# Kernel tuning notes

Measured on AMD Instinct MI355X. Metric: run time of the kernel, lower is better.

Reference implementation:

```python
import jax, jax.numpy as jnp
import numpy as np

K_HOPS = 2


def setup_inputs() -> dict:
    key = jax.random.key(0)
    k1, k2, k3 = jax.random.split(key, 3)
    N, E, D, C = 100000, 3200000, 512, 40
    x = jax.random.normal(k1, (N, D), dtype=jnp.float32)
    edge_index = jax.random.randint(k2, (2, E), 0, N, dtype=jnp.int64)
    W = jax.random.normal(k3, (C, D), dtype=jnp.float32) * 0.05
    b = jnp.zeros((C,), dtype=jnp.float32)
    return {"x": x, "edge_index": edge_index, "W": W, "b": b}


def reference(x, edge_index, W, b):
    # SGConv: K-hop symmetric-normalized propagation, then Linear, then log_softmax.
    # Dropout is identity at inference (training=False).
    N = x.shape[0]
    loop = jnp.arange(N, dtype=edge_index.dtype)
    src = jnp.concatenate([edge_index[0], loop])  # source nodes (+ self-loops)
    dst = jnp.concatenate([edge_index[1], loop])  # target nodes (+ self-loops)
    ew = jnp.ones(src.shape[0], dtype=x.dtype)
    # deg^{-1/2} A_hat deg^{-1/2}: degree computed at the target (col) index, as in PyG gcn_norm
    deg = jax.ops.segment_sum(ew, dst, num_segments=N)
    dinv = jnp.where(deg > 0, jax.lax.rsqrt(deg), 0.0)
    norm = dinv[src] * dinv[dst]  # [E+N]
    h = x
    for _ in range(K_HOPS):
        # gather source features, weight, scatter-add to targets
        h = jax.ops.segment_sum(norm[:, None] * h[src], dst, num_segments=N)
    logits = h @ W.T + b  # [N, C]
    return jax.nn.log_softmax(logits, axis=1)
```

## Files before the change

### kernel.cpp

```cpp
#include <hip/hip_runtime.h>
#include <hip/hip_bf16.h>


#define TPB 256
#define ETILE 16384

typedef __attribute__((ext_vector_type(8))) short short8v;
typedef __attribute__((ext_vector_type(4))) float f32x4;

__device__ inline short f2bf(float f) {
    unsigned u = __float_as_uint(f);
    unsigned r = (u + 0x7fffu + ((u >> 16) & 1u)) >> 16;
    return (short)r;
}
__device__ inline float bf2f(short s) {
    return __uint_as_float(((unsigned)(unsigned short)s) << 16);
}

__global__ void k_wconv(const float* __restrict__ W, short* __restrict__ Wb,
                        int* __restrict__ bcnt, int nb) {
    if (blockIdx.x == 0)
        for (int i = threadIdx.x; i < nb; i += TPB) bcnt[i] = 0;
    int idx = blockIdx.x * TPB + threadIdx.x;
    int c = idx >> 9, k = idx & 511;
    float v = (c < 40) ? W[c * 512 + k] : 0.f;
    Wb[idx] = f2bf(v);
}

__global__ __launch_bounds__(TPB) void k_bhist(
    const int* __restrict__ dst, int* __restrict__ bcnt, int E, int nb) {
    __shared__ int h[512];
    int t = threadIdx.x;
    for (int i = t; i < nb; i += TPB) h[i] = 0;
    __syncthreads();
    int e0 = blockIdx.x * ETILE;
    int e1 = min(e0 + ETILE, E);
    for (int e = e0 + t; e < e1; e += TPB)
        atomicAdd(&h[dst[e] >> 8], 1);
    __syncthreads();
    for (int i = t; i < nb; i += TPB)
        if (h[i]) atomicAdd(&bcnt[i], h[i]);
}

__global__ __launch_bounds__(512) void k_boff(
    const int* __restrict__ bcnt, int* __restrict__ boff,
    int* __restrict__ bcur, int nb) {
    __shared__ int s[512];
    int t = threadIdx.x;
    int own = (t < nb) ? bcnt[t] : 0;
    s[t] = own;
    __syncthreads();
    for (int off = 1; off < 512; off <<= 1) {
        int v = (t >= off) ? s[t - off] : 0;
        __syncthreads();
        s[t] += v;
        __syncthreads();
    }
    if (t < nb) {
        int ex = s[t] - own;
        boff[t] = ex;
        bcur[t] = ex;
        if (t == nb - 1) boff[nb] = s[t];
    }
}

__global__ __launch_bounds__(TPB) void k_part(
    const int* __restrict__ src, const int* __restrict__ dst,
    int* __restrict__ bcur, int* __restrict__ pairs, int E, int nb) {
    __shared__ int hist[512], base[512];
    int t = threadIdx.x;
    for (int i = t; i < nb; i += TPB) hist[i] = 0;
    __syncthreads();
    int e0 = blockIdx.x * ETILE;
    int e1 = min(e0 + ETILE, E);
    for (int e = e0 + t; e < e1; e += TPB)
        atomicAdd(&hist[dst[e] >> 8], 1);
    __syncthreads();
    for (int i = t; i < nb; i += TPB) {
        base[i] = hist[i] ? atomicAdd(&bcur[i], hist[i]) : 0;
        hist[i] = 0;
    }
    __syncthreads();
    for (int e = e0 + t; e < e1; e += TPB) {
        int d = dst[e];
        int b = d >> 8;
        int pos = base[b] + atomicAdd(&hist[b], 1);
        pairs[pos] = ((d & 255) << 20) | src[e];
    }
}

__global__ __launch_bounds__(TPB) void k_sort(
    const int* __restrict__ pairs, const int* __restrict__ boff,
    int* __restrict__ csr, int* __restrict__ row_ptr, float* __restrict__ dinv,
    int N, int nb) {
    __shared__ int hist[256], excl[256], lcur[256];
    int b = blockIdx.x, t = threadIdx.x;
    hist[t] = 0;
    __syncthreads();
    int beg = boff[b], end = boff[b + 1];
    for (int j = beg + t; j < end; j += TPB)
        atomicAdd(&hist[pairs[j] >> 20], 1);
    __syncthreads();
    int own = hist[t];
    excl[t] = own;
    __syncthreads();
    for (int off = 1; off < 256; off <<= 1) {
        int v = (t >= off) ? excl[t - off] : 0;
        __syncthreads();
        excl[t] += v;
        __syncthreads();
    }
    int node = (b << 8) + t;
    if (node < N) {
        row_ptr[node] = beg + excl[t] - own;
        dinv[node] = rsqrtf((float)(own + 1));
    }
    lcur[t] = 0;
    __syncthreads();
    for (int j = beg + t; j < end; j += TPB) {
        int u = pairs[j];
        int dl = u >> 20;
        int pos = beg + (excl[dl] - hist[dl]) + atomicAdd(&lcur[dl], 1);
        csr[pos] = u & 0xFFFFF;
    }
    if (b == nb - 1 && t == 0) row_ptr[N] = end;
}

__global__ __launch_bounds__(TPB) void k_matmul_mfma(
    const float* __restrict__ x, const short* __restrict__ Wb,
    const float* __restrict__ dinv, short* __restrict__ z, int N) {
    int wid  = threadIdx.x >> 6;
    int lane = threadIdx.x & 63;
    int rbase = blockIdx.x * 64 + wid * 16;
    if (rbase >= N) return;
    int arow   = rbase + (lane & 15);
    int aclamp = min(arow, N - 1);
    int koff   = (lane >> 4) * 8;
    const float* xrow = x + (size_t)aclamp * 512 + koff;
    const short* wb   = Wb + (lane & 15) * 512 + koff;

    f32x4 acc0 = {0.f,0.f,0.f,0.f}, acc1 = {0.f,0.f,0.f,0.f}, acc2 = {0.f,0.f,0.f,0.f};
    for (int ks = 0; ks < 16; ++ks) {
        int k0 = ks * 32;
        float4 f0 = *reinterpret_cast<const float4*>(xrow + k0);
        float4 f1 = *reinterpret_cast<const float4*>(xrow + k0 + 4);
        short8v a;
        a[0] = f2bf(f0.x); a[1] = f2bf(f0.y); a[2] = f2bf(f0.z); a[3] = f2bf(f0.w);
        a[4] = f2bf(f1.x); a[5] = f2bf(f1.y); a[6] = f2bf(f1.z); a[7] = f2bf(f1.w);
        short8v b0 = *reinterpret_cast<const short8v*>(wb + k0);
        short8v b1 = *reinterpret_cast<const short8v*>(wb + 16 * 512 + k0);
        short8v b2 = *reinterpret_cast<const short8v*>(wb + 32 * 512 + k0);
        acc0 = __builtin_amdgcn_mfma_f32_16x16x32_bf16(a, b0, acc0, 0, 0, 0);
        acc1 = __builtin_amdgcn_mfma_f32_16x16x32_bf16(a, b1, acc1, 0, 0, 0);
        acc2 = __builtin_amdgcn_mfma_f32_16x16x32_bf16(a, b2, acc2, 0, 0, 0);
    }
    int col = lane & 15;
    int rw  = rbase + (lane >> 4) * 4;
#pragma unroll
    for (int reg = 0; reg < 4; ++reg) {
        int r = rw + reg;
        if (r < N) {
            float di = dinv[r];
            z[(size_t)r * 40 + col]      = f2bf(di * acc0[reg]);
            z[(size_t)r * 40 + 16 + col] = f2bf(di * acc1[reg]);
            if (col < 8)
                z[(size_t)r * 40 + 32 + col] = f2bf(di * acc2[reg]);
        }
    }
}

__device__ inline void gather_acc(
    const short8v* __restrict__ Z, const int* __restrict__ csr,
    int beg, int end, int c8, float acc[8]) {
    int j = beg;
    for (; j + 8 <= end; j += 8) {
        int s0 = csr[j],   s1 = csr[j+1], s2 = csr[j+2], s3 = csr[j+3];
        int s4 = csr[j+4], s5 = csr[j+5], s6 = csr[j+6], s7 = csr[j+7];
        short8v v0 = Z[s0 * 5 + c8];
        short8v v1 = Z[s1 * 5 + c8];
        short8v v2 = Z[s2 * 5 + c8];
        short8v v3 = Z[s3 * 5 + c8];
        short8v v4 = Z[s4 * 5 + c8];
        short8v v5 = Z[s5 * 5 + c8];
        short8v v6 = Z[s6 * 5 + c8];
        short8v v7 = Z[s7 * 5 + c8];
#pragma unroll
        for (int k = 0; k < 8; ++k)
            acc[k] += ((bf2f(v0[k]) + bf2f(v1[k])) + (bf2f(v2[k]) + bf2f(v3[k])))
                    + ((bf2f(v4[k]) + bf2f(v5[k])) + (bf2f(v6[k]) + bf2f(v7[k])));
    }
    for (; j + 4 <= end; j += 4) {
        int s0 = csr[j], s1 = csr[j+1], s2 = csr[j+2], s3 = csr[j+3];
        short8v v0 = Z[s0 * 5 + c8];
        short8v v1 = Z[s1 * 5 + c8];
        short8v v2 = Z[s2 * 5 + c8];
        short8v v3 = Z[s3 * 5 + c8];
#pragma unroll
        for (int k = 0; k < 8; ++k)
            acc[k] += (bf2f(v0[k]) + bf2f(v1[k])) + (bf2f(v2[k]) + bf2f(v3[k]));
    }
    for (; j < end; ++j) {
        short8v v = Z[csr[j] * 5 + c8];
#pragma unroll
        for (int k = 0; k < 8; ++k) acc[k] += bf2f(v[k]);
    }
}

__global__ __launch_bounds__(TPB) void k_hop1(
    const int* __restrict__ csr, const int* __restrict__ row_ptr,
    const float* __restrict__ dinv, const short* __restrict__ zin,
    short* __restrict__ zout, int N) {
    int t = blockIdx.x * TPB + threadIdx.x;
    int node = t / 5;
    int c8 = t - node * 5;
    if (node >= N) return;
    const short8v* Z = reinterpret_cast<const short8v*>(zin);
    short8v sv = Z[node * 5 + c8];
    float acc[8];
#pragma unroll
    for (int k = 0; k < 8; ++k) acc[k] = bf2f(sv[k]);
    gather_acc(Z, csr, row_ptr[node], row_ptr[node + 1], c8, acc);
    float dd = dinv[node];
    float sc = dd * dd;
    short8v o;
#pragma unroll
    for (int k = 0; k < 8; ++k) o[k] = f2bf(sc * acc[k]);
    reinterpret_cast<short8v*>(zout)[node * 5 + c8] = o;
}

__global__ __launch_bounds__(TPB) void k_hop2_lsm(
    const int* __restrict__ csr, const int* __restrict__ row_ptr,
    const float* __restrict__ dinv, const short* __restrict__ zin,
    const float* __restrict__ bias, float* __restrict__ out, int N) {
    int wid  = threadIdx.x >> 6;
    int lane = threadIdx.x & 63;
    int g    = lane / 5;
    int c8   = lane - g * 5;
    int node = (blockIdx.x * 4 + wid) * 12 + g;
    bool active = (g < 12) && (node < N);

    float v[8];
    float lm = -1e30f;
    if (active) {
        const short8v* Z = reinterpret_cast<const short8v*>(zin);
        short8v sv = Z[node * 5 + c8];
        float acc[8];
#pragma unroll
        for (int k = 0; k < 8; ++k) acc[k] = bf2f(sv[k]);
        gather_acc(Z, csr, row_ptr[node], row_ptr[node + 1], c8, acc);
        float dd = dinv[node];
#pragma unroll
        for (int k = 0; k < 8; ++k) {
            v[k] = dd * acc[k] + bias[c8 * 8 + k];
            lm = fmaxf(lm, v[k]);
        }
    }
    int base = g * 5;
    float gm = lm;
#pragma unroll
    for (int k = 0; k < 5; ++k) gm = fmaxf(gm, __shfl(lm, base + k, 64));
    float ls = 0.f;
    if (active) {
#pragma unroll
        for (int k = 0; k < 8; ++k) ls += __expf(v[k] - gm);
    }
    float tot = 0.f;
#pragma unroll
    for (int k = 0; k < 5; ++k) tot += __shfl(ls, base + k, 64);
    if (active) {
        float lse = gm + __logf(tot);
        float* op = out + (size_t)node * 40 + c8 * 8;
        *reinterpret_cast<float4*>(op)     = make_float4(v[0]-lse, v[1]-lse, v[2]-lse, v[3]-lse);
        *reinterpret_cast<float4*>(op + 4) = make_float4(v[4]-lse, v[5]-lse, v[6]-lse, v[7]-lse);
    }
}

extern "C" void kernel_launch(void* const* d_in, const int* in_sizes, int n_in,
                              void* d_out, int out_size, void* d_ws, size_t ws_size,
                              hipStream_t stream) {
    const float* x  = (const float*)d_in[0];
    const int*   ei = (const int*)d_in[1];
    const float* W  = (const float*)d_in[2];
    const float* b  = (const float*)d_in[3];
    float* out = (float*)d_out;

    const int N = in_sizes[0] / 512;
    const int E = in_sizes[1] / 2;
    const int* src = ei;
    const int* dst = ei + E;
    const int nb = (N + 255) >> 8;

    short* z0b     = (short*)d_ws;
    short* z1b     = z0b + (size_t)N * 40;
    int*   csr     = (int*)(z1b + (size_t)N * 40);
    int*   pairs   = csr + E;
    int*   bcnt    = pairs + E;
    int*   boff    = bcnt + nb;
    int*   bcur    = boff + nb + 1;
    int*   row_ptr = bcur + nb;
    float* dinv    = (float*)(row_ptr + N + 1);
    short* Wb      = (short*)(dinv + N);

    int gT  = (E + ETILE - 1) / ETILE;
    int gM  = (N + 63) / 64;
    int gH1 = (N * 5 + TPB - 1) / TPB;
    int gH2 = (N + 47) / 48;

    k_wconv<<<(48 * 512) / TPB, TPB, 0, stream>>>(W, Wb, bcnt, nb);
    k_bhist<<<gT, TPB, 0, stream>>>(dst, bcnt, E, nb);
    k_boff<<<1, 512, 0, stream>>>(bcnt, boff, bcur, nb);
    k_part<<<gT, TPB, 0, stream>>>(src, dst, bcur, pairs, E, nb);
    k_sort<<<nb, TPB, 0, stream>>>(pairs, boff, csr, row_ptr, dinv, N, nb);

    k_matmul_mfma<<<gM, TPB, 0, stream>>>(x, Wb, dinv, z0b, N);

    k_hop1<<<gH1, TPB, 0, stream>>>(csr, row_ptr, dinv, z0b, z1b, N);
    k_hop2_lsm<<<gH2, TPB, 0, stream>>>(csr, row_ptr, dinv, z1b, b, out, N);
}
```

Baseline: 318.8 us.

## Pad bf16 feature rows to 64 columns and use 8 lanes per node

The bf16 propagated features are stored with a 64-element (128-byte) row stride instead of 40, so each node's row is aligned. Hop kernels now map 8 lanes per node with shift/mask indexing, and log-softmax reductions use xor shuffles within each 8-lane group. The pairs buffer is aliased onto the z1 region to save workspace, and the 8-way unrolled gather is removed. The cost is 60% more lanes and bytes per gathered row, including three idle lanes per node that still perform gather loads of zero padding.

```diff
diff --git a/kernel.cpp b/kernel.cpp
--- a/kernel.cpp
+++ b/kernel.cpp
@@ -4,6 +4,7 @@
 
 #define TPB 256
 #define ETILE 16384
+#define ZS 64
 
 typedef __attribute__((ext_vector_type(8))) short short8v;
 typedef __attribute__((ext_vector_type(4))) float f32x4;
@@ -161,10 +162,11 @@
         int r = rw + reg;
         if (r < N) {
             float di = dinv[r];
-            z[(size_t)r * 40 + col]      = f2bf(di * acc0[reg]);
-            z[(size_t)r * 40 + 16 + col] = f2bf(di * acc1[reg]);
-            if (col < 8)
-                z[(size_t)r * 40 + 32 + col] = f2bf(di * acc2[reg]);
+            short* zr = z + (size_t)r * ZS;
+            zr[col]      = f2bf(di * acc0[reg]);
+            zr[16 + col] = f2bf(di * acc1[reg]);
+            zr[32 + col] = f2bf(di * acc2[reg]);
+            zr[48 + col] = 0;
         }
     }
 }
@@ -173,34 +175,18 @@
     const short8v* __restrict__ Z, const int* __restrict__ csr,
     int beg, int end, int c8, float acc[8]) {
     int j = beg;
-    for (; j + 8 <= end; j += 8) {
-        int s0 = csr[j],   s1 = csr[j+1], s2 = csr[j+2], s3 = csr[j+3];
-        int s4 = csr[j+4], s5 = csr[j+5], s6 = csr[j+6], s7 = csr[j+7];
-        short8v v0 = Z[s0 * 5 + c8];
-        short8v v1 = Z[s1 * 5 + c8];
-        short8v v2 = Z[s2 * 5 + c8];
-        short8v v3 = Z[s3 * 5 + c8];
-        short8v v4 = Z[s4 * 5 + c8];
-        short8v v5 = Z[s5 * 5 + c8];
-        short8v v6 = Z[s6 * 5 + c8];
-        short8v v7 = Z[s7 * 5 + c8];
-#pragma unroll
-        for (int k = 0; k < 8; ++k)
-            acc[k] += ((bf2f(v0[k]) + bf2f(v1[k])) + (bf2f(v2[k]) + bf2f(v3[k])))
-                    + ((bf2f(v4[k]) + bf2f(v5[k])) + (bf2f(v6[k]) + bf2f(v7[k])));
-    }
     for (; j + 4 <= end; j += 4) {
         int s0 = csr[j], s1 = csr[j+1], s2 = csr[j+2], s3 = csr[j+3];
-        short8v v0 = Z[s0 * 5 + c8];
-        short8v v1 = Z[s1 * 5 + c8];
-        short8v v2 = Z[s2 * 5 + c8];
-        short8v v3 = Z[s3 * 5 + c8];
+        short8v v0 = Z[s0 * 8 + c8];
+        short8v v1 = Z[s1 * 8 + c8];
+        short8v v2 = Z[s2 * 8 + c8];
+        short8v v3 = Z[s3 * 8 + c8];
 #pragma unroll
         for (int k = 0; k < 8; ++k)
             acc[k] += (bf2f(v0[k]) + bf2f(v1[k])) + (bf2f(v2[k]) + bf2f(v3[k]));
     }
     for (; j < end; ++j) {
-        short8v v = Z[csr[j] * 5 + c8];
+        short8v v = Z[csr[j] * 8 + c8];
 #pragma unroll
         for (int k = 0; k < 8; ++k) acc[k] += bf2f(v[k]);
     }
@@ -211,11 +197,11 @@
     const float* __restrict__ dinv, const short* __restrict__ zin,
     short* __restrict__ zout, int N) {
     int t = blockIdx.x * TPB + threadIdx.x;
-    int node = t / 5;
-    int c8 = t - node * 5;
+    int node = t >> 3;
+    int c8 = t & 7;
     if (node >= N) return;
     const short8v* Z = reinterpret_cast<const short8v*>(zin);
-    short8v sv = Z[node * 5 + c8];
+    short8v sv = Z[node * 8 + c8];
     float acc[8];
 #pragma unroll
     for (int k = 0; k < 8; ++k) acc[k] = bf2f(sv[k]);
@@ -225,50 +211,49 @@
     short8v o;
 #pragma unroll
     for (int k = 0; k < 8; ++k) o[k] = f2bf(sc * acc[k]);
-    reinterpret_cast<short8v*>(zout)[node * 5 + c8] = o;
+    reinterpret_cast<short8v*>(zout)[node * 8 + c8] = o;
 }
 
 __global__ __launch_bounds__(TPB) void k_hop2_lsm(
     const int* __restrict__ csr, const int* __restrict__ row_ptr,
     const float* __restrict__ dinv, const short* __restrict__ zin,
     const float* __restrict__ bias, float* __restrict__ out, int N) {
-    int wid  = threadIdx.x >> 6;
-    int lane = threadIdx.x & 63;
-    int g    = lane / 5;
-    int c8   = lane - g * 5;
-    int node = (blockIdx.x * 4 + wid) * 12 + g;
-    bool active = (g < 12) && (node < N);
+    int t = blockIdx.x * TPB + threadIdx.x;
+    int node = t >> 3;
+    int c8 = t & 7;
+    if (node >= N) return;
+    const short8v* Z = reinterpret_cast<const short8v*>(zin);
+    short8v sv = Z[node * 8 + c8];
+    float acc[8];
+#pragma unroll
+    for (int k = 0; k < 8; ++k) acc[k] = bf2f(sv[k]);
+    gather_acc(Z, csr, row_ptr[node], row_ptr[node + 1], c8, acc);
+    float dd = dinv[node];
 
     float v[8];
     float lm = -1e30f;
-    if (active) {
-        const short8v* Z = reinterpret_cast<const short8v*>(zin);
-        short8v sv = Z[node * 5 + c8];
-        float acc[8];
-#pragma unroll
-        for (int k = 0; k < 8; ++k) acc[k] = bf2f(sv[k]);
-        gather_acc(Z, csr, row_ptr[node], row_ptr[node + 1], c8, acc);
-        float dd = dinv[node];
+    bool live = (c8 < 5);
+    if (live) {
 #pragma unroll
         for (int k = 0; k < 8; ++k) {
             v[k] = dd * acc[k] + bias[c8 * 8 + k];
             lm = fmaxf(lm, v[k]);
         }
     }
-    int base = g * 5;
     float gm = lm;
-#pragma unroll
-    for (int k = 0; k < 5; ++k) gm = fmaxf(gm, __shfl(lm, base + k, 64));
+    gm = fmaxf(gm, __shfl_xor(gm, 1));
+    gm = fmaxf(gm, __shfl_xor(gm, 2));
+    gm = fmaxf(gm, __shfl_xor(gm, 4));
     float ls = 0.f;
-    if (active) {
+    if (live) {
 #pragma unroll
         for (int k = 0; k < 8; ++k) ls += __expf(v[k] - gm);
     }
-    float tot = 0.f;
-#pragma unroll
-    for (int k = 0; k < 5; ++k) tot += __shfl(ls, base + k, 64);
-    if (active) {
-        float lse = gm + __logf(tot);
+    ls += __shfl_xor(ls, 1);
+    ls += __shfl_xor(ls, 2);
+    ls += __shfl_xor(ls, 4);
+    if (live) {
+        float lse = gm + __logf(ls);
         float* op = out + (size_t)node * 40 + c8 * 8;
         *reinterpret_cast<float4*>(op)     = make_float4(v[0]-lse, v[1]-lse, v[2]-lse, v[3]-lse);
         *reinterpret_cast<float4*>(op + 4) = make_float4(v[4]-lse, v[5]-lse, v[6]-lse, v[7]-lse);
@@ -290,11 +275,11 @@
     const int* dst = ei + E;
     const int nb = (N + 255) >> 8;
 
-    short* z0b     = (short*)d_ws;
-    short* z1b     = z0b + (size_t)N * 40;
-    int*   csr     = (int*)(z1b + (size_t)N * 40);
-    int*   pairs   = csr + E;
-    int*   bcnt    = pairs + E;
+    short* z0      = (short*)d_ws;
+    short* z1      = z0 + (size_t)N * ZS;
+    int*   pairs   = (int*)z1;
+    int*   csr     = (int*)(z1 + (size_t)N * ZS);
+    int*   bcnt    = csr + E;
     int*   boff    = bcnt + nb;
     int*   bcur    = boff + nb + 1;
     int*   row_ptr = bcur + nb;
@@ -303,8 +288,7 @@
 
     int gT  = (E + ETILE - 1) / ETILE;
     int gM  = (N + 63) / 64;
-    int gH1 = (N * 5 + TPB - 1) / TPB;
-    int gH2 = (N + 47) / 48;
+    int gH  = (N * 8 + TPB - 1) / TPB;
 
     k_wconv<<<(48 * 512) / TPB, TPB, 0, stream>>>(W, Wb, bcnt, nb);
     k_bhist<<<gT, TPB, 0, stream>>>(dst, bcnt, E, nb);
@@ -312,8 +296,8 @@
     k_part<<<gT, TPB, 0, stream>>>(src, dst, bcur, pairs, E, nb);
     k_sort<<<nb, TPB, 0, stream>>>(pairs, boff, csr, row_ptr, dinv, N, nb);
 
-    k_matmul_mfma<<<gM, TPB, 0, stream>>>(x, Wb, dinv, z0b, N);
-
-    k_hop1<<<gH1, TPB, 0, stream>>>(csr, row_ptr, dinv, z0b, z1b, N);
-    k_hop2_lsm<<<gH2, TPB, 0, stream>>>(csr, row_ptr, dinv, z1b, b, out, N);
-}
+    k_matmul_mfma<<<gM, TPB, 0, stream>>>(x, Wb, dinv, z0, N);
+
+    k_hop1<<<gH, TPB, 0, stream>>>(csr, row_ptr, dinv, z0, z1, N);
+    k_hop2_lsm<<<gH, TPB, 0, stream>>>(csr, row_ptr, dinv, z1, b, out, N);
+}
```

New measurement: 310.7 us. 1.03x faster.
